# Performance work log

Measured on AMD Instinct MI355X. Metric: run time of the kernel, lower is better.

Reference implementation:

```python
import jax, jax.numpy as jnp
import numpy as np
from jax.scipy.special import digamma, gammaln

NUM_CLASSES = 3
FOCAL_GAMMA = 2.0
LABEL_SMOOTHING = 0.1
EVIDENTIAL_W = 0.1
CONTRASTIVE_W = 0.1
BOUNDARY_W = 0.15
TRIPLET_W = 0.1
QUALITY_W = 0.1
TRIPLET_MARGIN = 1.5


def setup_inputs() -> dict:
    key = jax.random.key(0)
    k1, k2, k3 = jax.random.split(key, 3)
    B, D = 4096, 512
    logits = jax.random.normal(k1, (B, NUM_CLASSES), dtype=jnp.float32)
    targets = jax.random.randint(k2, (B,), 0, 3)
    features = jax.random.normal(k3, (B, D), dtype=jnp.float32)
    alpha = jax.random.uniform(jax.random.fold_in(key, 7), (B, NUM_CLASSES), dtype=jnp.float32)
    focal_alpha = jnp.array([1.0, 2.0, 1.5], dtype=jnp.float32)
    class_weights = jnp.array([1.0, 2.0, 1.5], dtype=jnp.float32)
    return {"logits": logits, "targets": targets, "features": features,
            "alpha": alpha, "epoch": 1, "focal_alpha": focal_alpha,
            "class_weights": class_weights}


def reference(logits, targets, features, alpha, epoch, focal_alpha, class_weights):
    B = logits.shape[0]
    C = NUM_CLASSES

    # ---- focal loss (label-smoothed CE, torch semantics) ----
    logp = jax.nn.log_softmax(logits, axis=1)                      # [B,C]
    nll = -jnp.take_along_axis(logp, targets[:, None], axis=1)[:, 0]
    ce_ls = (1.0 - LABEL_SMOOTHING) * nll + LABEL_SMOOTHING * (-logp.mean(axis=1))
    pt = jnp.exp(-ce_ls)
    focal = (focal_alpha[targets] * (1.0 - pt) ** FOCAL_GAMMA * ce_ls).mean()

    # ---- weighted CE (torch weighted mean: sum(w*nll)/sum(w)) ----
    w = class_weights[targets]
    ce = (w * nll).sum() / w.sum()

    # ---- enhanced boundary loss ----
    probs = jax.nn.softmax(logits, axis=1)
    real = targets == 0
    semi = targets == 1
    syn = targets == 2
    rb = jnp.where(real, probs[:, 1] + 0.6 * probs[:, 2], 0.0).sum()
    sb = jnp.where(syn, probs[:, 1] + 0.4 * probs[:, 0], 0.0).sum()
    mb = jnp.where(semi, 1.0 - probs[:, 1] + 0.3 * (probs[:, 0] + probs[:, 2]), 0.0).sum()
    boundary = (rb + sb + 4.5 * mb) / (B + 1e-8)

    total = 0.4 * focal + 0.3 * ce + BOUNDARY_W * boundary

    # ---- normalized features and pairwise cosine-sim matrix ----
    norms = jnp.linalg.norm(features, axis=1, keepdims=True)
    f = features / jnp.maximum(norms, 1e-12)
    sim = f @ f.T                                                  # [B,B]
    same = targets[:, None] == targets[None, :]
    eye = jnp.eye(B, dtype=bool)

    # ---- enhanced contrastive loss ----
    pos = jnp.where(same, (1.0 - sim) ** 2, 0.0).sum()
    neg = jnp.where(~same, jnp.clip(sim - 0.2, 0.0) ** 2, 0.0).sum()
    semi_pair = semi[:, None] & semi[None, :]
    semi_l = jnp.where(semi_pair, (1.0 - sim) ** 2, 0.0).sum()
    contrastive = (pos + neg + 4.0 * semi_l) / (B * B + 1e-8)

    # ---- enhanced triplet loss (batch-hard, vectorized) ----
    d2 = jnp.clip(2.0 - 2.0 * sim, 0.0)
    dist = jnp.sqrt(jnp.where(eye, 1.0, d2))  # diag masked; safe sqrt
    pos_mask = same & ~eye
    neg_mask = ~same
    hp = jnp.max(jnp.where(pos_mask, dist, -jnp.inf), axis=1)
    hn = jnp.min(jnp.where(neg_mask, dist, jnp.inf), axis=1)
    valid = pos_mask.any(axis=1) & neg_mask.any(axis=1)
    margin = TRIPLET_MARGIN * jnp.where(targets == 1, 2.5, 1.0)
    tl = jax.nn.relu(hp - hn + margin)
    cnt = valid.sum()
    triplet = jnp.where(cnt > 0,
                        jnp.where(valid, tl, 0.0).sum() / jnp.maximum(cnt, 1),
                        0.0)

    # ---- quality-invariant loss (upper-tri same-class pairs) ----
    upper = jnp.triu(jnp.ones((B, B), dtype=bool), k=1)
    qmask = same & upper
    npairs = qmask.sum()
    q = jnp.where(qmask, (1.0 - sim) ** 2, 0.0).sum() / jnp.maximum(npairs, 1)
    frac2 = syn.astype(jnp.float32).mean()
    q = q * jnp.where(syn.sum() > 0, 1.0 + 2.5 * frac2, 1.0)
    quality = jnp.where(npairs > 0, q, 0.0)

    # ---- evidential loss ----
    onehot = jax.nn.one_hot(targets, C, dtype=jnp.float32)
    S = alpha.sum(axis=1, keepdims=True) + 1e-8
    likelihood = (onehot * (digamma(S) - digamma(alpha + 1e-8))).sum(axis=1)
    at = onehot + (1.0 - onehot) * alpha
    ats = at.sum(axis=1) + 1e-8
    kl = (gammaln(ats) - gammaln(at + 1e-8).sum(axis=1)
          + ((at - 1.0) * (digamma(at + 1e-8) - digamma(ats[:, None] + 1e-8))).sum(axis=1))
    annealing = min(1.0, (epoch / 25.0) ** 2)
    evidential = likelihood.mean() + annealing * 0.2 * kl.mean()

    total = (total + CONTRASTIVE_W * contrastive + TRIPLET_W * triplet
             + QUALITY_W * quality + EVIDENTIAL_W * evidential)
    return total
```

## Files before the change

kernel.cpp:

```cpp
#include <hip/hip_runtime.h>
#include <hip/hip_bf16.h>
#include <cstdint>

#define NCLS 3

typedef __attribute__((ext_vector_type(8))) __bf16 bf8;
typedef __attribute__((ext_vector_type(4))) float f32x4;

#if defined(__has_builtin)
#if __has_builtin(__builtin_amdgcn_global_load_lds)
#define USE_GLL 1
#endif
#endif
#ifndef USE_GLL
#define USE_GLL 0
#endif

#if USE_GLL
__device__ __forceinline__ void gll16(const __bf16* g, __bf16* l){
  __builtin_amdgcn_global_load_lds(
      (const __attribute__((address_space(1))) void*)g,
      (__attribute__((address_space(3))) void*)l, 16, 0, 0);
}
#endif

__device__ __forceinline__ unsigned mapf(float x){
  unsigned u = __float_as_uint(x);
  return (u & 0x80000000u) ? ~u : (u | 0x80000000u);
}
__device__ __forceinline__ float unmapf(unsigned u){
  return __uint_as_float((u & 0x80000000u) ? (u & 0x7FFFFFFFu) : ~u);
}

__device__ float digammaf_(float x){
  float r = 0.f;
  while (x < 6.f){ r -= 1.f/x; x += 1.f; }
  float inv = 1.f/x, inv2 = inv*inv;
  r += logf(x) - 0.5f*inv
     - inv2*(0.08333333333f - inv2*(0.008333333333f - inv2*0.003968253968f));
  return r;
}

__global__ void k_init(float* acc, unsigned* cnts, unsigned* rowMinU, unsigned* rowMaxU, int B){
  int i = blockIdx.x*blockDim.x + threadIdx.x;
  if (i < B){ rowMinU[i] = 0xFFFFFFFFu; rowMaxU[i] = 0u; }
  if (i < 16) acc[i] = 0.f;
  if (i < NCLS) cnts[i] = 0u;
}

__global__ __launch_bounds__(256) void k_norm(const float* __restrict__ feat,
                                              __bf16* __restrict__ fb, int B, int D){
  int wave = threadIdx.x >> 6, lane = threadIdx.x & 63;
  int row = blockIdx.x*4 + wave;
  if (row >= B) return;
  const float* src = feat + (size_t)row*D;
  float ss = 0.f;
  for (int c = lane*4; c < D; c += 64*4){
    float4 v = *(const float4*)(src + c);
    ss += v.x*v.x + v.y*v.y + v.z*v.z + v.w*v.w;
  }
  #pragma unroll
  for (int off=32; off; off>>=1) ss += __shfl_xor(ss, off);
  float inv = 1.f / fmaxf(sqrtf(ss), 1e-12f);
  __bf16* dst = fb + (size_t)row*D;
  for (int c = lane*8; c < D; c += 64*8){
    float4 v0 = *(const float4*)(src + c);
    float4 v1 = *(const float4*)(src + c + 4);
    bf8 o;
    o[0]=(__bf16)(v0.x*inv); o[1]=(__bf16)(v0.y*inv);
    o[2]=(__bf16)(v0.z*inv); o[3]=(__bf16)(v0.w*inv);
    o[4]=(__bf16)(v1.x*inv); o[5]=(__bf16)(v1.y*inv);
    o[6]=(__bf16)(v1.z*inv); o[7]=(__bf16)(v1.w*inv);
    *(bf8*)(dst + c) = o;
  }
}

__global__ __launch_bounds__(256) void k_sample(const float* __restrict__ logits,
    const int* __restrict__ targets, const float* __restrict__ alpha,
    const float* __restrict__ fa, const float* __restrict__ cw,
    int B, float* acc, unsigned* cnts){
  int i = blockIdx.x*blockDim.x + threadIdx.x;
  float focal_i=0, ce_n=0, ce_d=0, bnd=0, lik=0, kl=0;
  int t = 0; bool active = i < B;
  if (active){
    float l0=logits[3*i], l1=logits[3*i+1], l2=logits[3*i+2];
    t = targets[i];
    float m = fmaxf(l0, fmaxf(l1,l2));
    float e0=expf(l0-m), e1=expf(l1-m), e2=expf(l2-m);
    float se = e0+e1+e2;
    float lse = m + logf(se);
    float lp0=l0-lse, lp1=l1-lse, lp2=l2-lse;
    float lpt = (t==0)?lp0:((t==1)?lp1:lp2);
    float nll = -lpt;
    float ce_ls = 0.9f*nll + 0.1f*(-(lp0+lp1+lp2)*(1.f/3.f));
    float pt = expf(-ce_ls);
    float om = 1.f - pt;
    focal_i = fa[t]*om*om*ce_ls;
    float w = cw[t];
    ce_n = w*nll; ce_d = w;
    float p0=e0/se, p1=e1/se, p2=e2/se;
    if (t==0)      bnd = p1 + 0.6f*p2;
    else if (t==2) bnd = p1 + 0.4f*p0;
    else           bnd = 4.5f*(1.f - p1 + 0.3f*(p0+p2));
    float a0=alpha[3*i], a1=alpha[3*i+1], a2=alpha[3*i+2];
    float S = a0+a1+a2 + 1e-8f;
    float at_ = (t==0)?a0:((t==1)?a1:a2);
    lik = digammaf_(S) - digammaf_(at_ + 1e-8f);
    float b0 = (t==0)?1.f:a0, b1 = (t==1)?1.f:a1, b2 = (t==2)?1.f:a2;
    float ats = b0+b1+b2 + 1e-8f;
    float psa = digammaf_(ats + 1e-8f);
    kl = lgammaf(ats)
       - (lgammaf(b0+1e-8f)+lgammaf(b1+1e-8f)+lgammaf(b2+1e-8f))
       + (b0-1.f)*(digammaf_(b0+1e-8f)-psa)
       + (b1-1.f)*(digammaf_(b1+1e-8f)-psa)
       + (b2-1.f)*(digammaf_(b2+1e-8f)-psa);
  }
  unsigned long long m0 = __ballot(active && t==0);
  unsigned long long m1 = __ballot(active && t==1);
  unsigned long long m2 = __ballot(active && t==2);
  #pragma unroll
  for (int off=32; off; off>>=1){
    focal_i += __shfl_xor(focal_i, off);
    ce_n    += __shfl_xor(ce_n, off);
    ce_d    += __shfl_xor(ce_d, off);
    bnd     += __shfl_xor(bnd, off);
    lik     += __shfl_xor(lik, off);
    kl      += __shfl_xor(kl, off);
  }
  if ((threadIdx.x & 63) == 0){
    atomicAdd(&acc[4], focal_i); atomicAdd(&acc[5], ce_n); atomicAdd(&acc[6], ce_d);
    atomicAdd(&acc[7], bnd);     atomicAdd(&acc[8], lik);  atomicAdd(&acc[9], kl);
    atomicAdd(&cnts[0], (unsigned)__popcll(m0));
    atomicAdd(&cnts[1], (unsigned)__popcll(m1));
    atomicAdd(&cnts[2], (unsigned)__popcll(m2));
  }
}

__global__ __launch_bounds__(256) void k_pairs(const __bf16* __restrict__ fb,
    const int* __restrict__ targets, int B, int D,
    float* acc, unsigned* rowMinU, unsigned* rowMaxU){
  __shared__ __bf16 sA[128*32];
  __shared__ __bf16 sB[128*32];
  __shared__ int sRT[128];
  __shared__ int sCT[128];
  __shared__ float sred[4][4];

  int t = blockIdx.x;
  int bx = (int)((sqrtf(8.f*(float)t + 1.f) - 1.f)*0.5f);
  while ((bx+1)*(bx+2)/2 <= t) bx++;
  while (bx*(bx+1)/2 > t) bx--;
  int by = t - bx*(bx+1)/2;
  bool isDiag = (by == bx);
  int rowBase = by*128, colBase = bx*128;

  int tid = threadIdx.x, lane = tid & 63, wave = tid >> 6;
  int wr = wave >> 1, wc = wave & 1;
  int quad = lane >> 4, l16 = lane & 15;

  if (tid < 128) sRT[tid] = targets[rowBase + tid];
  else           sCT[tid-128] = targets[colBase + tid - 128];

  const __bf16* gA[2]; const __bf16* gB[2];
  __bf16* lA[2]; __bf16* lB[2];
  #pragma unroll
  for (int rnd=0; rnd<2; rnd++){
    int e = tid*8 + rnd*2048;
    int row = e >> 5;
    int cb = (e & 31) >> 3;
    int gcb = cb ^ ((row >> 1) & 3);
    gA[rnd] = fb + (size_t)(rowBase + row)*D + gcb*8;
    gB[rnd] = fb + (size_t)(colBase + row)*D + gcb*8;
#if USE_GLL
    lA[rnd] = sA + wave*512 + rnd*2048;
    lB[rnd] = sB + wave*512 + rnd*2048;
#else
    lA[rnd] = sA + tid*8 + rnd*2048;
    lB[rnd] = sB + tid*8 + rnd*2048;
#endif
  }

  int offA[4], offB[4];
  #pragma unroll
  for (int mi=0; mi<4; mi++){
    int R = wr*64 + mi*16 + l16;
    offA[mi] = R*32 + ((quad ^ ((R>>1)&3))*8);
  }
  #pragma unroll
  for (int ni=0; ni<4; ni++){
    int R = wc*64 + ni*16 + l16;
    offB[ni] = R*32 + ((quad ^ ((R>>1)&3))*8);
  }

  f32x4 C[4][4] = {};

  for (int k0=0; k0<D; k0+=32){
    __syncthreads();
#if USE_GLL
    gll16(gA[0]+k0, lA[0]); gll16(gA[1]+k0, lA[1]);
    gll16(gB[0]+k0, lB[0]); gll16(gB[1]+k0, lB[1]);
#else
    *(bf8*)lA[0] = *(const bf8*)(gA[0]+k0);
    *(bf8*)lA[1] = *(const bf8*)(gA[1]+k0);
    *(bf8*)lB[0] = *(const bf8*)(gB[0]+k0);
    *(bf8*)lB[1] = *(const bf8*)(gB[1]+k0);
#endif
    __syncthreads();
    bf8 aF[4], bF[4];
    #pragma unroll
    for (int mi=0; mi<4; mi++) aF[mi] = *(const bf8*)(sA + offA[mi]);
    #pragma unroll
    for (int ni=0; ni<4; ni++) bF[ni] = *(const bf8*)(sB + offB[ni]);
    #pragma unroll
    for (int mi=0; mi<4; mi++)
      #pragma unroll
      for (int ni=0; ni<4; ni++)
        C[mi][ni] = __builtin_amdgcn_mfma_f32_16x16x32_bf16(aF[mi], bF[ni], C[mi][ni], 0,0,0);
  }

  int tcol[4];
  #pragma unroll
  for (int ni=0; ni<4; ni++) tcol[ni] = sCT[wc*64 + ni*16 + l16];

  float pos=0.f, neg=0.f, semi=0.f, diag=0.f;
  float cmin[4], cmax[4];
  #pragma unroll
  for (int ni=0; ni<4; ni++){ cmin[ni]=2.f; cmax[ni]=-2.f; }

  #pragma unroll
  for (int mi=0; mi<4; mi++){
    #pragma unroll
    for (int r=0; r<4; r++){
      int rl = wr*64 + mi*16 + quad*4 + r;
      int row = rowBase + rl;
      int tr = sRT[rl];
      float vmin = 2.f, vmax = -2.f;
      #pragma unroll
      for (int ni=0; ni<4; ni++){
        int col = colBase + wc*64 + ni*16 + l16;
        float s = C[mi][ni][r];
        if (tr == tcol[ni]){
          float om = 1.f - s;
          float q = om*om;
          pos += q;
          if (tr == 1) semi += q;
          if (row == col) diag += q;
          else {
            vmin = fminf(vmin, s);
            cmin[ni] = fminf(cmin[ni], s);
          }
        } else {
          float c0 = fmaxf(s - 0.2f, 0.f);
          neg += c0*c0;
          vmax = fmaxf(vmax, s);
          cmax[ni] = fmaxf(cmax[ni], s);
        }
      }
      #pragma unroll
      for (int off=1; off<16; off<<=1){
        vmin = fminf(vmin, __shfl_xor(vmin, off));
        vmax = fmaxf(vmax, __shfl_xor(vmax, off));
      }
      if (l16 == 0){
        atomicMin(&rowMinU[row], mapf(vmin));
        atomicMax(&rowMaxU[row], mapf(vmax));
      }
    }
  }

  if (!isDiag){
    #pragma unroll
    for (int ni=0; ni<4; ni++){
      float cn = cmin[ni], cx = cmax[ni];
      cn = fminf(cn, __shfl_xor(cn, 16)); cn = fminf(cn, __shfl_xor(cn, 32));
      cx = fmaxf(cx, __shfl_xor(cx, 16)); cx = fmaxf(cx, __shfl_xor(cx, 32));
      if (quad == 0){
        int col = colBase + wc*64 + ni*16 + l16;
        atomicMin(&rowMinU[col], mapf(cn));
        atomicMax(&rowMaxU[col], mapf(cx));
      }
    }
  }

  #pragma unroll
  for (int off=32; off; off>>=1){
    pos  += __shfl_xor(pos, off);
    neg  += __shfl_xor(neg, off);
    semi += __shfl_xor(semi, off);
    diag += __shfl_xor(diag, off);
  }
  if (lane == 0){ sred[wave][0]=pos; sred[wave][1]=neg; sred[wave][2]=semi; sred[wave][3]=diag; }
  __syncthreads();
  if (tid == 0){
    float fac = isDiag ? 1.f : 2.f;
    float p=0,n=0,s2=0,d=0;
    for (int w2=0; w2<4; w2++){ p+=sred[w2][0]; n+=sred[w2][1]; s2+=sred[w2][2]; d+=sred[w2][3]; }
    atomicAdd(&acc[0], p*fac); atomicAdd(&acc[1], n*fac);
    atomicAdd(&acc[2], s2*fac); atomicAdd(&acc[3], d);
  }
}

__global__ __launch_bounds__(256) void k_final(const int* __restrict__ targets,
    const int* __restrict__ epoch_p, int B, const float* acc, const unsigned* cnts,
    const unsigned* rowMinU, const unsigned* rowMaxU, float* out){
  int n0 = (int)cnts[0], n1 = (int)cnts[1], n2 = (int)cnts[2];
  float tsum = 0.f; float tcnt = 0.f;
  for (int i = threadIdx.x; i < B; i += 256){
    int t = targets[i];
    int nt = (t==0)?n0:((t==1)?n1:n2);
    if (nt - 1 > 0 && B - nt > 0){
      float mn = unmapf(rowMinU[i]);
      float mx = unmapf(rowMaxU[i]);
      float hp = sqrtf(fmaxf(2.f - 2.f*mn, 0.f));
      float hn = sqrtf(fmaxf(2.f - 2.f*mx, 0.f));
      float margin = 1.5f * ((t==1) ? 2.5f : 1.f);
      float tl = fmaxf(hp - hn + margin, 0.f);
      tsum += tl; tcnt += 1.f;
    }
  }
  #pragma unroll
  for (int off=32; off; off>>=1){ tsum += __shfl_xor(tsum, off); tcnt += __shfl_xor(tcnt, off); }
  __shared__ float sb[4][2];
  int wave = threadIdx.x>>6, lane = threadIdx.x&63;
  if (lane==0){ sb[wave][0]=tsum; sb[wave][1]=tcnt; }
  __syncthreads();
  if (threadIdx.x==0){
    float ts=0, tn=0;
    for (int w2=0;w2<4;w2++){ ts+=sb[w2][0]; tn+=sb[w2][1]; }
    float triplet = (tn > 0.f) ? ts / fmaxf(tn, 1.f) : 0.f;
    float pos=acc[0], neg=acc[1], semi=acc[2], diag=acc[3];
    float Bf = (float)B;
    float focal = acc[4] / Bf;
    float ce = acc[5] / acc[6];
    float boundary = acc[7] / (Bf + 1e-8f);
    float contrastive = (pos + neg + 4.f*semi) / (Bf*Bf + 1e-8f);
    long long npl = ((long long)n0*(n0-1) + (long long)n1*(n1-1) + (long long)n2*(n2-1))/2;
    float qsum = (pos - diag) * 0.5f;
    float q = qsum / (float)(npl > 0 ? npl : 1);
    if (n2 > 0) q *= (1.f + 2.5f * ((float)n2 / Bf));
    float quality = (npl > 0) ? q : 0.f;
    int ep = epoch_p[0];
    float er = (float)ep / 25.f;
    float ann = fminf(1.f, er*er);
    float evidential = acc[8]/Bf + ann*0.2f*acc[9]/Bf;
    float total = 0.4f*focal + 0.3f*ce + 0.15f*boundary
                + 0.1f*contrastive + 0.1f*triplet + 0.1f*quality + 0.1f*evidential;
    out[0] = total;
  }
}

extern "C" void kernel_launch(void* const* d_in, const int* in_sizes, int n_in,
                              void* d_out, int out_size, void* d_ws, size_t ws_size,
                              hipStream_t stream){
  const float* logits   = (const float*)d_in[0];
  const int*   targets  = (const int*)d_in[1];
  const float* features = (const float*)d_in[2];
  const float* alpha    = (const float*)d_in[3];
  const int*   epoch    = (const int*)d_in[4];
  const float* fa       = (const float*)d_in[5];
  const float* cw       = (const float*)d_in[6];
  int B = in_sizes[1];
  int D = in_sizes[2] / B;

  char* ws = (char*)d_ws;
  float*    acc     = (float*)ws;
  unsigned* cnts    = (unsigned*)(ws + 64);
  unsigned* rowMinU = (unsigned*)(ws + 128);
  unsigned* rowMaxU = (unsigned*)(ws + 128 + (size_t)B*4);
  __bf16*   fb      = (__bf16*)(ws + 128 + (size_t)B*8);

  k_init  <<<(B+255)/256, 256, 0, stream>>>(acc, cnts, rowMinU, rowMaxU, B);
  k_norm  <<<(B+3)/4,     256, 0, stream>>>(features, fb, B, D);
  k_sample<<<(B+255)/256, 256, 0, stream>>>(logits, targets, alpha, fa, cw, B, acc, cnts);
  int ntile = B/128;
  int nblk  = ntile*(ntile+1)/2;
  k_pairs <<<nblk, 256, 0, stream>>>(fb, targets, B, D, acc, rowMinU, rowMaxU);
  k_final <<<1, 256, 0, stream>>>(targets, epoch, B, acc, cnts, rowMinU, rowMaxU, (float*)d_out);
}
```

Before: 147.5 us.

## Fuse init/norm/sample kernels and double-buffer LDS tiles in pair GEMM

Merges the init, normalization and per-sample loss kernels into one prep kernel. Per-wave partial sums now go to slots that the final kernel reduces, in place of global atomics. The pair kernel double-buffers its shared-memory tiles so the next K-slice loads while MFMAs run on the current one, which drops one barrier per iteration. This cuts launch overhead and atomic contention at the cost of twice the LDS, which may lower occupancy.

```diff
diff --git a/kernel.cpp b/kernel.cpp
--- a/kernel.cpp
+++ b/kernel.cpp
@@ -1,8 +1,6 @@
 #include <hip/hip_runtime.h>
 #include <hip/hip_bf16.h>
 #include <cstdint>
-
-#define NCLS 3
 
 typedef __attribute__((ext_vector_type(8))) __bf16 bf8;
 typedef __attribute__((ext_vector_type(4))) float f32x4;
@@ -41,83 +39,83 @@
   return r;
 }
 
-__global__ void k_init(float* acc, unsigned* cnts, unsigned* rowMinU, unsigned* rowMaxU, int B){
-  int i = blockIdx.x*blockDim.x + threadIdx.x;
-  if (i < B){ rowMinU[i] = 0xFFFFFFFFu; rowMaxU[i] = 0u; }
-  if (i < 16) acc[i] = 0.f;
-  if (i < NCLS) cnts[i] = 0u;
-}
-
-__global__ __launch_bounds__(256) void k_norm(const float* __restrict__ feat,
-                                              __bf16* __restrict__ fb, int B, int D){
-  int wave = threadIdx.x >> 6, lane = threadIdx.x & 63;
-  int row = blockIdx.x*4 + wave;
-  if (row >= B) return;
-  const float* src = feat + (size_t)row*D;
-  float ss = 0.f;
-  for (int c = lane*4; c < D; c += 64*4){
-    float4 v = *(const float4*)(src + c);
-    ss += v.x*v.x + v.y*v.y + v.z*v.z + v.w*v.w;
-  }
-  #pragma unroll
-  for (int off=32; off; off>>=1) ss += __shfl_xor(ss, off);
-  float inv = 1.f / fmaxf(sqrtf(ss), 1e-12f);
-  __bf16* dst = fb + (size_t)row*D;
-  for (int c = lane*8; c < D; c += 64*8){
-    float4 v0 = *(const float4*)(src + c);
-    float4 v1 = *(const float4*)(src + c + 4);
-    bf8 o;
-    o[0]=(__bf16)(v0.x*inv); o[1]=(__bf16)(v0.y*inv);
-    o[2]=(__bf16)(v0.z*inv); o[3]=(__bf16)(v0.w*inv);
-    o[4]=(__bf16)(v1.x*inv); o[5]=(__bf16)(v1.y*inv);
-    o[6]=(__bf16)(v1.z*inv); o[7]=(__bf16)(v1.w*inv);
-    *(bf8*)(dst + c) = o;
-  }
-}
-
-__global__ __launch_bounds__(256) void k_sample(const float* __restrict__ logits,
-    const int* __restrict__ targets, const float* __restrict__ alpha,
-    const float* __restrict__ fa, const float* __restrict__ cw,
-    int B, float* acc, unsigned* cnts){
-  int i = blockIdx.x*blockDim.x + threadIdx.x;
-  float focal_i=0, ce_n=0, ce_d=0, bnd=0, lik=0, kl=0;
-  int t = 0; bool active = i < B;
-  if (active){
-    float l0=logits[3*i], l1=logits[3*i+1], l2=logits[3*i+2];
-    t = targets[i];
-    float m = fmaxf(l0, fmaxf(l1,l2));
-    float e0=expf(l0-m), e1=expf(l1-m), e2=expf(l2-m);
-    float se = e0+e1+e2;
-    float lse = m + logf(se);
-    float lp0=l0-lse, lp1=l1-lse, lp2=l2-lse;
-    float lpt = (t==0)?lp0:((t==1)?lp1:lp2);
-    float nll = -lpt;
-    float ce_ls = 0.9f*nll + 0.1f*(-(lp0+lp1+lp2)*(1.f/3.f));
-    float pt = expf(-ce_ls);
-    float om = 1.f - pt;
-    focal_i = fa[t]*om*om*ce_ls;
-    float w = cw[t];
-    ce_n = w*nll; ce_d = w;
-    float p0=e0/se, p1=e1/se, p2=e2/se;
-    if (t==0)      bnd = p1 + 0.6f*p2;
-    else if (t==2) bnd = p1 + 0.4f*p0;
-    else           bnd = 4.5f*(1.f - p1 + 0.3f*(p0+p2));
-    float a0=alpha[3*i], a1=alpha[3*i+1], a2=alpha[3*i+2];
-    float S = a0+a1+a2 + 1e-8f;
-    float at_ = (t==0)?a0:((t==1)?a1:a2);
-    lik = digammaf_(S) - digammaf_(at_ + 1e-8f);
-    float b0 = (t==0)?1.f:a0, b1 = (t==1)?1.f:a1, b2 = (t==2)?1.f:a2;
-    float ats = b0+b1+b2 + 1e-8f;
-    float psa = digammaf_(ats + 1e-8f);
-    kl = lgammaf(ats)
-       - (lgammaf(b0+1e-8f)+lgammaf(b1+1e-8f)+lgammaf(b2+1e-8f))
-       + (b0-1.f)*(digammaf_(b0+1e-8f)-psa)
-       + (b1-1.f)*(digammaf_(b1+1e-8f)-psa)
-       + (b2-1.f)*(digammaf_(b2+1e-8f)-psa);
-  }
-  unsigned long long m0 = __ballot(active && t==0);
-  unsigned long long m1 = __ballot(active && t==1);
-  unsigned long long m2 = __ballot(active && t==2);
+__global__ __launch_bounds__(256) void k_prep(const float* __restrict__ feat,
+    __bf16* __restrict__ fb,
+    const float* __restrict__ logits, const int* __restrict__ targets,
+    const float* __restrict__ alpha,  const float* __restrict__ fa,
+    const float* __restrict__ cw, int B, int D,
+    float* __restrict__ psum, unsigned* __restrict__ pcnt,
+    float* __restrict__ acc, unsigned* rowMinU, unsigned* rowMaxU){
+  int bid = blockIdx.x, tid = threadIdx.x;
+  int wave = tid >> 6, lane = tid & 63;
+
+  int row = bid*4 + wave;
+  if (row < B){
+    const float* src = feat + (size_t)row*D;
+    float ss = 0.f;
+    for (int c = lane*4; c < D; c += 64*4){
+      float4 v = *(const float4*)(src + c);
+      ss += v.x*v.x + v.y*v.y + v.z*v.z + v.w*v.w;
+    }
+    #pragma unroll
+    for (int off=32; off; off>>=1) ss += __shfl_xor(ss, off);
+    float inv = 1.f / fmaxf(sqrtf(ss), 1e-12f);
+    __bf16* dst = fb + (size_t)row*D;
+    for (int c = lane*8; c < D; c += 64*8){
+      float4 v0 = *(const float4*)(src + c);
+      float4 v1 = *(const float4*)(src + c + 4);
+      bf8 o;
+      o[0]=(__bf16)(v0.x*inv); o[1]=(__bf16)(v0.y*inv);
+      o[2]=(__bf16)(v0.z*inv); o[3]=(__bf16)(v0.w*inv);
+      o[4]=(__bf16)(v1.x*inv); o[5]=(__bf16)(v1.y*inv);
+      o[6]=(__bf16)(v1.z*inv); o[7]=(__bf16)(v1.w*inv);
+      *(bf8*)(dst + c) = o;
+    }
+  }
+
+  int SB = B >> 8;
+  if (bid == SB && tid < 16) acc[tid] = 0.f;
+  if (bid >= SB) return;
+
+  int i = bid*256 + tid;
+  rowMinU[i] = 0xFFFFFFFFu; rowMaxU[i] = 0u;
+
+  float l0=logits[3*i], l1=logits[3*i+1], l2=logits[3*i+2];
+  int t = targets[i];
+  float m = fmaxf(l0, fmaxf(l1,l2));
+  float e0=expf(l0-m), e1=expf(l1-m), e2=expf(l2-m);
+  float se = e0+e1+e2;
+  float lse = m + logf(se);
+  float lp0=l0-lse, lp1=l1-lse, lp2=l2-lse;
+  float lpt = (t==0)?lp0:((t==1)?lp1:lp2);
+  float nll = -lpt;
+  float ce_ls = 0.9f*nll + 0.1f*(-(lp0+lp1+lp2)*(1.f/3.f));
+  float pt = expf(-ce_ls);
+  float om = 1.f - pt;
+  float focal_i = fa[t]*om*om*ce_ls;
+  float w = cw[t];
+  float ce_n = w*nll, ce_d = w;
+  float p0=e0/se, p1=e1/se, p2=e2/se;
+  float bnd;
+  if (t==0)      bnd = p1 + 0.6f*p2;
+  else if (t==2) bnd = p1 + 0.4f*p0;
+  else           bnd = 4.5f*(1.f - p1 + 0.3f*(p0+p2));
+  float a0=alpha[3*i], a1=alpha[3*i+1], a2=alpha[3*i+2];
+  float S = a0+a1+a2 + 1e-8f;
+  float at_ = (t==0)?a0:((t==1)?a1:a2);
+  float lik = digammaf_(S) - digammaf_(at_ + 1e-8f);
+  float b0 = (t==0)?1.f:a0, b1 = (t==1)?1.f:a1, b2 = (t==2)?1.f:a2;
+  float ats = b0+b1+b2 + 1e-8f;
+  float psa = digammaf_(ats + 1e-8f);
+  float kl = lgammaf(ats)
+     - (lgammaf(b0+1e-8f)+lgammaf(b1+1e-8f)+lgammaf(b2+1e-8f))
+     + (b0-1.f)*(digammaf_(b0+1e-8f)-psa)
+     + (b1-1.f)*(digammaf_(b1+1e-8f)-psa)
+     + (b2-1.f)*(digammaf_(b2+1e-8f)-psa);
+
+  unsigned long long m0 = __ballot(t==0);
+  unsigned long long m1 = __ballot(t==1);
+  unsigned long long m2 = __ballot(t==2);
   #pragma unroll
   for (int off=32; off; off>>=1){
     focal_i += __shfl_xor(focal_i, off);
@@ -127,20 +125,21 @@
     lik     += __shfl_xor(lik, off);
     kl      += __shfl_xor(kl, off);
   }
-  if ((threadIdx.x & 63) == 0){
-    atomicAdd(&acc[4], focal_i); atomicAdd(&acc[5], ce_n); atomicAdd(&acc[6], ce_d);
-    atomicAdd(&acc[7], bnd);     atomicAdd(&acc[8], lik);  atomicAdd(&acc[9], kl);
-    atomicAdd(&cnts[0], (unsigned)__popcll(m0));
-    atomicAdd(&cnts[1], (unsigned)__popcll(m1));
-    atomicAdd(&cnts[2], (unsigned)__popcll(m2));
+  if (lane == 0){
+    int slot = bid*4 + wave;
+    psum[slot*8+0]=focal_i; psum[slot*8+1]=ce_n; psum[slot*8+2]=ce_d;
+    psum[slot*8+3]=bnd;     psum[slot*8+4]=lik;  psum[slot*8+5]=kl;
+    pcnt[slot*4+0]=(unsigned)__popcll(m0);
+    pcnt[slot*4+1]=(unsigned)__popcll(m1);
+    pcnt[slot*4+2]=(unsigned)__popcll(m2);
   }
 }
 
 __global__ __launch_bounds__(256) void k_pairs(const __bf16* __restrict__ fb,
     const int* __restrict__ targets, int B, int D,
     float* acc, unsigned* rowMinU, unsigned* rowMaxU){
-  __shared__ __bf16 sA[128*32];
-  __shared__ __bf16 sB[128*32];
+  __shared__ __bf16 sA[2][4096];
+  __shared__ __bf16 sB[2][4096];
   __shared__ int sRT[128];
   __shared__ int sCT[128];
   __shared__ float sred[4][4];
@@ -161,23 +160,16 @@
   else           sCT[tid-128] = targets[colBase + tid - 128];
 
   const __bf16* gA[2]; const __bf16* gB[2];
-  __bf16* lA[2]; __bf16* lB[2];
-  #pragma unroll
-  for (int rnd=0; rnd<2; rnd++){
-    int e = tid*8 + rnd*2048;
+  #pragma unroll
+  for (int r=0; r<2; r++){
+    int e = tid*8 + r*2048;
     int row = e >> 5;
     int cb = (e & 31) >> 3;
     int gcb = cb ^ ((row >> 1) & 3);
-    gA[rnd] = fb + (size_t)(rowBase + row)*D + gcb*8;
-    gB[rnd] = fb + (size_t)(colBase + row)*D + gcb*8;
-#if USE_GLL
-    lA[rnd] = sA + wave*512 + rnd*2048;
-    lB[rnd] = sB + wave*512 + rnd*2048;
-#else
-    lA[rnd] = sA + tid*8 + rnd*2048;
-    lB[rnd] = sB + tid*8 + rnd*2048;
-#endif
-  }
+    gA[r] = fb + (size_t)(rowBase + row)*D + gcb*8;
+    gB[r] = fb + (size_t)(colBase + row)*D + gcb*8;
+  }
+  int wofs = wave*512;
 
   int offA[4], offB[4];
   #pragma unroll
@@ -191,30 +183,54 @@
     offB[ni] = R*32 + ((quad ^ ((R>>1)&3))*8);
   }
 
+#if USE_GLL
+  #pragma unroll
+  for (int r=0; r<2; r++){
+    gll16(gA[r], &sA[0][wofs + r*2048]);
+    gll16(gB[r], &sB[0][wofs + r*2048]);
+  }
+#else
+  #pragma unroll
+  for (int r=0; r<2; r++){
+    *(bf8*)&sA[0][tid*8 + r*2048] = *(const bf8*)gA[r];
+    *(bf8*)&sB[0][tid*8 + r*2048] = *(const bf8*)gB[r];
+  }
+#endif
+
   f32x4 C[4][4] = {};
-
-  for (int k0=0; k0<D; k0+=32){
+  int NIT = D/32;
+  int cur = 0;
+
+  for (int it=0; it<NIT; ++it){
     __syncthreads();
+    if (it+1 < NIT){
+      int k0 = (it+1)*32;
+      int nb = cur ^ 1;
 #if USE_GLL
-    gll16(gA[0]+k0, lA[0]); gll16(gA[1]+k0, lA[1]);
-    gll16(gB[0]+k0, lB[0]); gll16(gB[1]+k0, lB[1]);
+      #pragma unroll
+      for (int r=0; r<2; r++){
+        gll16(gA[r]+k0, &sA[nb][wofs + r*2048]);
+        gll16(gB[r]+k0, &sB[nb][wofs + r*2048]);
+      }
 #else
-    *(bf8*)lA[0] = *(const bf8*)(gA[0]+k0);
-    *(bf8*)lA[1] = *(const bf8*)(gA[1]+k0);
-    *(bf8*)lB[0] = *(const bf8*)(gB[0]+k0);
-    *(bf8*)lB[1] = *(const bf8*)(gB[1]+k0);
-#endif
-    __syncthreads();
+      #pragma unroll
+      for (int r=0; r<2; r++){
+        *(bf8*)&sA[nb][tid*8 + r*2048] = *(const bf8*)(gA[r]+k0);
+        *(bf8*)&sB[nb][tid*8 + r*2048] = *(const bf8*)(gB[r]+k0);
+      }
+#endif
+    }
     bf8 aF[4], bF[4];
     #pragma unroll
-    for (int mi=0; mi<4; mi++) aF[mi] = *(const bf8*)(sA + offA[mi]);
-    #pragma unroll
-    for (int ni=0; ni<4; ni++) bF[ni] = *(const bf8*)(sB + offB[ni]);
+    for (int mi=0; mi<4; mi++) aF[mi] = *(const bf8*)(&sA[cur][offA[mi]]);
+    #pragma unroll
+    for (int ni=0; ni<4; ni++) bF[ni] = *(const bf8*)(&sB[cur][offB[ni]]);
     #pragma unroll
     for (int mi=0; mi<4; mi++)
       #pragma unroll
       for (int ni=0; ni<4; ni++)
         C[mi][ni] = __builtin_amdgcn_mfma_f32_16x16x32_bf16(aF[mi], bF[ni], C[mi][ni], 0,0,0);
+    cur ^= 1;
   }
 
   int tcol[4];
@@ -239,8 +255,8 @@
         int col = colBase + wc*64 + ni*16 + l16;
         float s = C[mi][ni][r];
         if (tr == tcol[ni]){
-          float om = 1.f - s;
-          float q = om*om;
+          float omv = 1.f - s;
+          float q = omv*omv;
           pos += q;
           if (tr == 1) semi += q;
           if (row == col) diag += q;
@@ -300,11 +316,38 @@
 }
 
 __global__ __launch_bounds__(256) void k_final(const int* __restrict__ targets,
-    const int* __restrict__ epoch_p, int B, const float* acc, const unsigned* cnts,
+    const int* __restrict__ epoch_p, int B, int SB,
+    const float* acc, const float* psum, const unsigned* pcnt,
     const unsigned* rowMinU, const unsigned* rowMaxU, float* out){
-  int n0 = (int)cnts[0], n1 = (int)cnts[1], n2 = (int)cnts[2];
-  float tsum = 0.f; float tcnt = 0.f;
-  for (int i = threadIdx.x; i < B; i += 256){
+  __shared__ float tot[6];
+  __shared__ unsigned cn[3];
+  int tid = threadIdx.x;
+  int nslots = SB*4;
+
+  if (tid < 64){
+    float v0=0,v1=0,v2=0,v3=0,v4=0,v5=0;
+    int c0=0,c1=0,c2=0;
+    for (int s=tid; s<nslots; s+=64){
+      v0+=psum[s*8+0]; v1+=psum[s*8+1]; v2+=psum[s*8+2];
+      v3+=psum[s*8+3]; v4+=psum[s*8+4]; v5+=psum[s*8+5];
+      c0+=(int)pcnt[s*4+0]; c1+=(int)pcnt[s*4+1]; c2+=(int)pcnt[s*4+2];
+    }
+    #pragma unroll
+    for (int off=32; off; off>>=1){
+      v0+=__shfl_xor(v0,off); v1+=__shfl_xor(v1,off); v2+=__shfl_xor(v2,off);
+      v3+=__shfl_xor(v3,off); v4+=__shfl_xor(v4,off); v5+=__shfl_xor(v5,off);
+      c0+=__shfl_xor(c0,off); c1+=__shfl_xor(c1,off); c2+=__shfl_xor(c2,off);
+    }
+    if (tid == 0){
+      tot[0]=v0; tot[1]=v1; tot[2]=v2; tot[3]=v3; tot[4]=v4; tot[5]=v5;
+      cn[0]=(unsigned)c0; cn[1]=(unsigned)c1; cn[2]=(unsigned)c2;
+    }
+  }
+  __syncthreads();
+  int n0=(int)cn[0], n1=(int)cn[1], n2=(int)cn[2];
+
+  float tsum = 0.f, tcnt = 0.f;
+  for (int i = tid; i < B; i += 256){
     int t = targets[i];
     int nt = (t==0)?n0:((t==1)?n1:n2);
     if (nt - 1 > 0 && B - nt > 0){
@@ -320,18 +363,18 @@
   #pragma unroll
   for (int off=32; off; off>>=1){ tsum += __shfl_xor(tsum, off); tcnt += __shfl_xor(tcnt, off); }
   __shared__ float sb[4][2];
-  int wave = threadIdx.x>>6, lane = threadIdx.x&63;
+  int wave = tid>>6, lane = tid&63;
   if (lane==0){ sb[wave][0]=tsum; sb[wave][1]=tcnt; }
   __syncthreads();
-  if (threadIdx.x==0){
+  if (tid==0){
     float ts=0, tn=0;
     for (int w2=0;w2<4;w2++){ ts+=sb[w2][0]; tn+=sb[w2][1]; }
     float triplet = (tn > 0.f) ? ts / fmaxf(tn, 1.f) : 0.f;
     float pos=acc[0], neg=acc[1], semi=acc[2], diag=acc[3];
     float Bf = (float)B;
-    float focal = acc[4] / Bf;
-    float ce = acc[5] / acc[6];
-    float boundary = acc[7] / (Bf + 1e-8f);
+    float focal = tot[0] / Bf;
+    float ce = tot[1] / tot[2];
+    float boundary = tot[3] / (Bf + 1e-8f);
     float contrastive = (pos + neg + 4.f*semi) / (Bf*Bf + 1e-8f);
     long long npl = ((long long)n0*(n0-1) + (long long)n1*(n1-1) + (long long)n2*(n2-1))/2;
     float qsum = (pos - diag) * 0.5f;
@@ -341,7 +384,7 @@
     int ep = epoch_p[0];
     float er = (float)ep / 25.f;
     float ann = fminf(1.f, er*er);
-    float evidential = acc[8]/Bf + ann*0.2f*acc[9]/Bf;
+    float evidential = tot[4]/Bf + ann*0.2f*tot[5]/Bf;
     float total = 0.4f*focal + 0.3f*ce + 0.15f*boundary
                 + 0.1f*contrastive + 0.1f*triplet + 0.1f*quality + 0.1f*evidential;
     out[0] = total;
@@ -360,19 +403,21 @@
   const float* cw       = (const float*)d_in[6];
   int B = in_sizes[1];
   int D = in_sizes[2] / B;
+  int SB = B >> 8;
 
   char* ws = (char*)d_ws;
   float*    acc     = (float*)ws;
-  unsigned* cnts    = (unsigned*)(ws + 64);
-  unsigned* rowMinU = (unsigned*)(ws + 128);
-  unsigned* rowMaxU = (unsigned*)(ws + 128 + (size_t)B*4);
-  __bf16*   fb      = (__bf16*)(ws + 128 + (size_t)B*8);
-
-  k_init  <<<(B+255)/256, 256, 0, stream>>>(acc, cnts, rowMinU, rowMaxU, B);
-  k_norm  <<<(B+3)/4,     256, 0, stream>>>(features, fb, B, D);
-  k_sample<<<(B+255)/256, 256, 0, stream>>>(logits, targets, alpha, fa, cw, B, acc, cnts);
+  unsigned* pcnt    = (unsigned*)(ws + 128);
+  float*    psum    = (float*)(ws + 128 + (size_t)SB*64);
+  unsigned* rowMinU = (unsigned*)(ws + 4096);
+  unsigned* rowMaxU = (unsigned*)(ws + 4096 + (size_t)B*4);
+  __bf16*   fb      = (__bf16*)(ws + 4096 + (size_t)B*8);
+
+  k_prep <<<B/4, 256, 0, stream>>>(features, fb, logits, targets, alpha, fa, cw,
+                                   B, D, psum, pcnt, acc, rowMinU, rowMaxU);
   int ntile = B/128;
   int nblk  = ntile*(ntile+1)/2;
-  k_pairs <<<nblk, 256, 0, stream>>>(fb, targets, B, D, acc, rowMinU, rowMaxU);
-  k_final <<<1, 256, 0, stream>>>(targets, epoch, B, acc, cnts, rowMinU, rowMaxU, (float*)d_out);
-}
+  k_pairs<<<nblk, 256, 0, stream>>>(fb, targets, B, D, acc, rowMinU, rowMaxU);
+  k_final<<<1, 256, 0, stream>>>(targets, epoch, B, SB, acc, psum, pcnt,
+                                 rowMinU, rowMaxU, (float*)d_out);
+}
```

Result: faster. 138.1 us (-6.4%).
